# Kernel tuning notes

Hardware: AMD Instinct MI355X
Metric: run time of the kernel (lower is better)

Reference implementation:

```python
import jax, jax.numpy as jnp
import numpy as np

EPS = 1e-9

def setup_inputs() -> dict:
    key = jax.random.key(0)
    k1, k2 = jax.random.split(key)
    h = jax.random.normal(k1, (16384, 4096), dtype=jnp.float32)
    W = jax.random.normal(k2, (64, 4096), dtype=jnp.float32) * 0.02  # nn.Linear weight [n_experts, d]
    return {"h": h, "W": W}

def reference(h, W):
    k = 2
    # logits: [tokens, n_experts]
    logits = jnp.einsum('td,ed->te', h, W)
    weights_full = jax.nn.softmax(logits, axis=-1)
    # top-k on logits (torch.topk returns sorted descending, as does lax.top_k)
    _, idx = jax.lax.top_k(logits, k)  # idx: [tokens, k]
    # masked renormalization: since top-k indices are distinct, the masked sum
    # equals the sum of gathered softmax weights
    gathered = jnp.take_along_axis(weights_full, idx, axis=-1)  # [tokens, k]
    weights_topk = gathered / (jnp.sum(gathered, axis=-1, keepdims=True) + EPS)
    return weights_topk, idx
```

## Files before the change

### kernel.cpp

```cpp
#include <hip/hip_runtime.h>
#include <math.h>

#define DIM   4096
#define NEXP  64
#define MB    32
#define KC    128
#define NST   (DIM / KC)
#define ASTR  (KC + 8)

typedef _Float16 f16x8 __attribute__((ext_vector_type(8)));
typedef _Float16 f16x4 __attribute__((ext_vector_type(4)));
typedef float    f32x4 __attribute__((ext_vector_type(4)));

__global__ __launch_bounds__(256)
void convert_w_kernel(const float* __restrict__ W,
                      _Float16* __restrict__ wh, _Float16* __restrict__ wl) {
    int i = (blockIdx.x * 256 + threadIdx.x) * 4;
    float4 v = *(const float4*)(W + i);
    _Float16 a0 = (_Float16)v.x, a1 = (_Float16)v.y;
    _Float16 a2 = (_Float16)v.z, a3 = (_Float16)v.w;
    f16x4 hh = {a0, a1, a2, a3};
    f16x4 ll = {(_Float16)(v.x - (float)a0), (_Float16)(v.y - (float)a1),
                (_Float16)(v.z - (float)a2), (_Float16)(v.w - (float)a3)};
    *(f16x4*)(wh + i) = hh;
    *(f16x4*)(wl + i) = ll;
}

__global__ __launch_bounds__(256, 2)
void gate_mfma_kernel(const float* __restrict__ h,
                      const _Float16* __restrict__ wh,
                      const _Float16* __restrict__ wl,
                      float* __restrict__ out, int n_tokens) {
    __shared__ _Float16 Ah[2][MB][ASTR];
    __shared__ _Float16 Al[2][MB][ASTR];
    __shared__ float    lg[MB][NEXP + 4];

    const int tid  = threadIdx.x;
    const int lane = tid & 63;
    const int wv   = __builtin_amdgcn_readfirstlane(tid >> 6);
    const int mg   = wv & 1;
    const int ng   = wv >> 1;
    const int t0   = blockIdx.x * MB;
    const int l15  = lane & 15;
    const int quad = lane >> 4;

    const _Float16* bh0 = wh + (size_t)(32 * ng + l15) * DIM + 8 * quad;
    const _Float16* bh1 = bh0 + (size_t)16 * DIM;
    const _Float16* bl0 = wl + (size_t)(32 * ng + l15) * DIM + 8 * quad;
    const _Float16* bl1 = bl0 + (size_t)16 * DIM;

    f32x4 acc0 = {0.f, 0.f, 0.f, 0.f};
    f32x4 acc1 = {0.f, 0.f, 0.f, 0.f};

    float4 st[4];
    int s_t[4], s_q[4];
#pragma unroll
    for (int r = 0; r < 4; ++r) {
        int flat = r * 256 + tid;
        s_t[r] = flat >> 5;
        s_q[r] = flat & 31;
        st[r] = *(const float4*)(h + (size_t)(t0 + s_t[r]) * DIM + 4 * s_q[r]);
    }

    for (int c = 0; c < NST; ++c) {
        const int buf = c & 1;
#pragma unroll
        for (int r = 0; r < 4; ++r) {
            float4 v = st[r];
            _Float16 a0 = (_Float16)v.x, a1 = (_Float16)v.y;
            _Float16 a2 = (_Float16)v.z, a3 = (_Float16)v.w;
            f16x4 hh = {a0, a1, a2, a3};
            f16x4 ll = {(_Float16)(v.x - (float)a0), (_Float16)(v.y - (float)a1),
                        (_Float16)(v.z - (float)a2), (_Float16)(v.w - (float)a3)};
            *(f16x4*)(&Ah[buf][s_t[r]][4 * s_q[r]]) = hh;
            *(f16x4*)(&Al[buf][s_t[r]][4 * s_q[r]]) = ll;
        }
        __syncthreads();

        if (c + 1 < NST) {
            const int kn = (c + 1) * KC;
#pragma unroll
            for (int r = 0; r < 4; ++r)
                st[r] = *(const float4*)(h + (size_t)(t0 + s_t[r]) * DIM + kn + 4 * s_q[r]);
        }

        const _Float16* arow_h = &Ah[buf][16 * mg + l15][8 * quad];
        const _Float16* arow_l = &Al[buf][16 * mg + l15][8 * quad];
        const size_t kb = (size_t)c * KC;
#pragma unroll
        for (int s = 0; s < 4; ++s) {
            f16x8 af_h = *(const f16x8*)(arow_h + 32 * s);
            f16x8 af_l = *(const f16x8*)(arow_l + 32 * s);
            f16x8 b0h  = *(const f16x8*)(bh0 + kb + 32 * s);
            f16x8 b1h  = *(const f16x8*)(bh1 + kb + 32 * s);
            f16x8 b0l  = *(const f16x8*)(bl0 + kb + 32 * s);
            f16x8 b1l  = *(const f16x8*)(bl1 + kb + 32 * s);
            acc0 = __builtin_amdgcn_mfma_f32_16x16x32_f16(af_h, b0h, acc0, 0, 0, 0);
            acc0 = __builtin_amdgcn_mfma_f32_16x16x32_f16(af_h, b0l, acc0, 0, 0, 0);
            acc0 = __builtin_amdgcn_mfma_f32_16x16x32_f16(af_l, b0h, acc0, 0, 0, 0);
            acc1 = __builtin_amdgcn_mfma_f32_16x16x32_f16(af_h, b1h, acc1, 0, 0, 0);
            acc1 = __builtin_amdgcn_mfma_f32_16x16x32_f16(af_h, b1l, acc1, 0, 0, 0);
            acc1 = __builtin_amdgcn_mfma_f32_16x16x32_f16(af_l, b1h, acc1, 0, 0, 0);
        }
    }

#pragma unroll
    for (int r = 0; r < 4; ++r) {
        lg[16 * mg + 4 * quad + r][32 * ng + l15]      = acc0[r];
        lg[16 * mg + 4 * quad + r][32 * ng + 16 + l15] = acc1[r];
    }
    __syncthreads();

    if (tid < MB) {
        const float* row = lg[tid];
        float m = -INFINITY;
#pragma unroll 8
        for (int e = 0; e < NEXP; ++e) m = fmaxf(m, row[e]);
        float z = 0.0f, b1 = -INFINITY, b2 = -INFINITY;
        int i1 = 0, i2 = 0;
        for (int e = 0; e < NEXP; ++e) {
            float v = row[e];
            z += expf(v - m);
            if (v > b1)      { b2 = b1; i2 = i1; b1 = v; i1 = e; }
            else if (v > b2) { b2 = v; i2 = e; }
        }
        float g1 = expf(b1 - m), g2 = expf(b2 - m);
        float w1 = g1 / z, w2 = g2 / z;
        float ssum = w1 + w2 + 1e-9f;
        int t = t0 + tid;
        *(float2*)(out + 2 * t) = make_float2(w1 / ssum, w2 / ssum);
        *(float2*)(out + 2 * n_tokens + 2 * t) = make_float2((float)i1, (float)i2);
    }
}

extern "C" void kernel_launch(void* const* d_in, const int* in_sizes, int n_in,
                              void* d_out, int out_size, void* d_ws, size_t ws_size,
                              hipStream_t stream) {
    const float* h = (const float*)d_in[0];
    const float* W = (const float*)d_in[1];
    float* out = (float*)d_out;
    const int n_tokens = in_sizes[0] / DIM;

    _Float16* wh = (_Float16*)d_ws;
    _Float16* wl = wh + (size_t)NEXP * DIM;

    convert_w_kernel<<<(NEXP * DIM) / (256 * 4), 256, 0, stream>>>(W, wh, wl);
    gate_mfma_kernel<<<n_tokens / MB, 256, 0, stream>>>(h, wh, wl, out, n_tokens);
}
```

Before: 435.4 us.

## Pre-pack W into MFMA fragment order, swizzle LDS, and prefetch B fragments

The weight-conversion kernel now writes W's fp16 hi/lo split in MFMA fragment order, so each lane's B load is one contiguous coalesced 16-byte read. Those fragments are double-buffered in registers one K-chunk ahead. The LDS A tiles drop row padding in favour of an XOR swizzle to avoid bank conflicts. The warp split changes so each wave owns 16 experts and both 16-token M tiles, and occupancy is raised to 3 blocks per CU. The cost is more register pressure from the prefetched B fragments and the unroll, which could limit the higher occupancy target.

Result: faster. 371.6 us (-14.6%).

```diff
diff --git a/kernel.cpp b/kernel.cpp
--- a/kernel.cpp
+++ b/kernel.cpp
@@ -6,74 +6,88 @@
 #define MB    32
 #define KC    128
 #define NST   (DIM / KC)
-#define ASTR  (KC + 8)
 
 typedef _Float16 f16x8 __attribute__((ext_vector_type(8)));
 typedef _Float16 f16x4 __attribute__((ext_vector_type(4)));
 typedef float    f32x4 __attribute__((ext_vector_type(4)));
 
 __global__ __launch_bounds__(256)
-void convert_w_kernel(const float* __restrict__ W,
-                      _Float16* __restrict__ wh, _Float16* __restrict__ wl) {
-    int i = (blockIdx.x * 256 + threadIdx.x) * 4;
-    float4 v = *(const float4*)(W + i);
-    _Float16 a0 = (_Float16)v.x, a1 = (_Float16)v.y;
-    _Float16 a2 = (_Float16)v.z, a3 = (_Float16)v.w;
-    f16x4 hh = {a0, a1, a2, a3};
-    f16x4 ll = {(_Float16)(v.x - (float)a0), (_Float16)(v.y - (float)a1),
-                (_Float16)(v.z - (float)a2), (_Float16)(v.w - (float)a3)};
-    *(f16x4*)(wh + i) = hh;
-    *(f16x4*)(wl + i) = ll;
+void pack_w_kernel(const float* __restrict__ W,
+                   _Float16* __restrict__ wph, _Float16* __restrict__ wpl) {
+    const int flat = blockIdx.x * 256 + threadIdx.x;
+    const int lane = flat & 63;
+    const int ck   = (flat >> 6) & 127;
+    const int nt   = flat >> 13;
+    const int e    = nt * 16 + (lane & 15);
+    const int k0   = ck * 32 + (lane >> 4) * 8;
+    const float* src = W + ((size_t)e << 12) + k0;
+    float4 v0 = *(const float4*)(src);
+    float4 v1 = *(const float4*)(src + 4);
+    float vv[8] = {v0.x, v0.y, v0.z, v0.w, v1.x, v1.y, v1.z, v1.w};
+    f16x8 hi, lo;
+#pragma unroll
+    for (int i = 0; i < 8; ++i) {
+        _Float16 hh = (_Float16)vv[i];
+        hi[i] = hh;
+        lo[i] = (_Float16)(vv[i] - (float)hh);
+    }
+    *(f16x8*)(wph + (size_t)flat * 8) = hi;
+    *(f16x8*)(wpl + (size_t)flat * 8) = lo;
 }
 
-__global__ __launch_bounds__(256, 2)
+__global__ __launch_bounds__(256, 3)
 void gate_mfma_kernel(const float* __restrict__ h,
-                      const _Float16* __restrict__ wh,
-                      const _Float16* __restrict__ wl,
+                      const _Float16* __restrict__ wph,
+                      const _Float16* __restrict__ wpl,
                       float* __restrict__ out, int n_tokens) {
-    __shared__ _Float16 Ah[2][MB][ASTR];
-    __shared__ _Float16 Al[2][MB][ASTR];
+    __shared__ _Float16 Ah[2][MB * KC];
+    __shared__ _Float16 Al[2][MB * KC];
     __shared__ float    lg[MB][NEXP + 4];
 
     const int tid  = threadIdx.x;
     const int lane = tid & 63;
     const int wv   = __builtin_amdgcn_readfirstlane(tid >> 6);
-    const int mg   = wv & 1;
-    const int ng   = wv >> 1;
-    const int t0   = blockIdx.x * MB;
     const int l15  = lane & 15;
     const int quad = lane >> 4;
+    const int t0   = blockIdx.x * MB;
 
-    const _Float16* bh0 = wh + (size_t)(32 * ng + l15) * DIM + 8 * quad;
-    const _Float16* bh1 = bh0 + (size_t)16 * DIM;
-    const _Float16* bl0 = wl + (size_t)(32 * ng + l15) * DIM + 8 * quad;
-    const _Float16* bl1 = bl0 + (size_t)16 * DIM;
-
-    f32x4 acc0 = {0.f, 0.f, 0.f, 0.f};
-    f32x4 acc1 = {0.f, 0.f, 0.f, 0.f};
-
+    int s_t[4], s_q[4];
     float4 st[4];
-    int s_t[4], s_q[4];
 #pragma unroll
     for (int r = 0; r < 4; ++r) {
         int flat = r * 256 + tid;
         s_t[r] = flat >> 5;
         s_q[r] = flat & 31;
-        st[r] = *(const float4*)(h + (size_t)(t0 + s_t[r]) * DIM + 4 * s_q[r]);
+        st[r]  = *(const float4*)(h + (size_t)(t0 + s_t[r]) * DIM + 4 * s_q[r]);
     }
 
+    const _Float16* bph = wph + ((size_t)(wv * 128) * 64 + lane) * 8;
+    const _Float16* bpl = wpl + ((size_t)(wv * 128) * 64 + lane) * 8;
+    f16x8 Bh[2][4], Bl[2][4];
+#pragma unroll
+    for (int s = 0; s < 4; ++s) {
+        Bh[0][s] = *(const f16x8*)(bph + s * 512);
+        Bl[0][s] = *(const f16x8*)(bpl + s * 512);
+    }
+
+    f32x4 acc0 = {0.f, 0.f, 0.f, 0.f};
+    f32x4 acc1 = {0.f, 0.f, 0.f, 0.f};
+
+#pragma unroll 2
     for (int c = 0; c < NST; ++c) {
         const int buf = c & 1;
 #pragma unroll
         for (int r = 0; r < 4; ++r) {
             float4 v = st[r];
-            _Float16 a0 = (_Float16)v.x, a1 = (_Float16)v.y;
-            _Float16 a2 = (_Float16)v.z, a3 = (_Float16)v.w;
+            _Float16 a0 = (_Float16)v.x, a1 = (_Float16)v.y,
+                     a2 = (_Float16)v.z, a3 = (_Float16)v.w;
             f16x4 hh = {a0, a1, a2, a3};
             f16x4 ll = {(_Float16)(v.x - (float)a0), (_Float16)(v.y - (float)a1),
                         (_Float16)(v.z - (float)a2), (_Float16)(v.w - (float)a3)};
-            *(f16x4*)(&Ah[buf][s_t[r]][4 * s_q[r]]) = hh;
-            *(f16x4*)(&Al[buf][s_t[r]][4 * s_q[r]]) = ll;
+            int t = s_t[r], q = s_q[r];
+            int addr = t * KC + (((q >> 1) ^ (t & 15)) << 3) + ((q & 1) << 2);
+            *(f16x4*)(&Ah[buf][addr]) = hh;
+            *(f16x4*)(&Al[buf][addr]) = ll;
         }
         __syncthreads();
 
@@ -82,32 +96,36 @@
 #pragma unroll
             for (int r = 0; r < 4; ++r)
                 st[r] = *(const float4*)(h + (size_t)(t0 + s_t[r]) * DIM + kn + 4 * s_q[r]);
+            const int nb = (c + 1) & 1;
+            const size_t coff = (size_t)(c + 1) * 4 * 512;
+#pragma unroll
+            for (int s = 0; s < 4; ++s) {
+                Bh[nb][s] = *(const f16x8*)(bph + coff + s * 512);
+                Bl[nb][s] = *(const f16x8*)(bpl + coff + s * 512);
+            }
         }
 
-        const _Float16* arow_h = &Ah[buf][16 * mg + l15][8 * quad];
-        const _Float16* arow_l = &Al[buf][16 * mg + l15][8 * quad];
-        const size_t kb = (size_t)c * KC;
 #pragma unroll
         for (int s = 0; s < 4; ++s) {
-            f16x8 af_h = *(const f16x8*)(arow_h + 32 * s);
-            f16x8 af_l = *(const f16x8*)(arow_l + 32 * s);
-            f16x8 b0h  = *(const f16x8*)(bh0 + kb + 32 * s);
-            f16x8 b1h  = *(const f16x8*)(bh1 + kb + 32 * s);
-            f16x8 b0l  = *(const f16x8*)(bl0 + kb + 32 * s);
-            f16x8 b1l  = *(const f16x8*)(bl1 + kb + 32 * s);
-            acc0 = __builtin_amdgcn_mfma_f32_16x16x32_f16(af_h, b0h, acc0, 0, 0, 0);
-            acc0 = __builtin_amdgcn_mfma_f32_16x16x32_f16(af_h, b0l, acc0, 0, 0, 0);
-            acc0 = __builtin_amdgcn_mfma_f32_16x16x32_f16(af_l, b0h, acc0, 0, 0, 0);
-            acc1 = __builtin_amdgcn_mfma_f32_16x16x32_f16(af_h, b1h, acc1, 0, 0, 0);
-            acc1 = __builtin_amdgcn_mfma_f32_16x16x32_f16(af_h, b1l, acc1, 0, 0, 0);
-            acc1 = __builtin_amdgcn_mfma_f32_16x16x32_f16(af_l, b1h, acc1, 0, 0, 0);
+            const int pb = (((4 * s + quad) ^ l15) << 3);
+            f16x8 a0h = *(const f16x8*)(&Ah[buf][l15 * KC + pb]);
+            f16x8 a1h = *(const f16x8*)(&Ah[buf][(16 + l15) * KC + pb]);
+            f16x8 a0l = *(const f16x8*)(&Al[buf][l15 * KC + pb]);
+            f16x8 a1l = *(const f16x8*)(&Al[buf][(16 + l15) * KC + pb]);
+            f16x8 bh = Bh[buf][s], bl = Bl[buf][s];
+            acc0 = __builtin_amdgcn_mfma_f32_16x16x32_f16(a0h, bh, acc0, 0, 0, 0);
+            acc1 = __builtin_amdgcn_mfma_f32_16x16x32_f16(a1h, bh, acc1, 0, 0, 0);
+            acc0 = __builtin_amdgcn_mfma_f32_16x16x32_f16(a0l, bh, acc0, 0, 0, 0);
+            acc1 = __builtin_amdgcn_mfma_f32_16x16x32_f16(a1l, bh, acc1, 0, 0, 0);
+            acc0 = __builtin_amdgcn_mfma_f32_16x16x32_f16(a0h, bl, acc0, 0, 0, 0);
+            acc1 = __builtin_amdgcn_mfma_f32_16x16x32_f16(a1h, bl, acc1, 0, 0, 0);
         }
     }
 
 #pragma unroll
     for (int r = 0; r < 4; ++r) {
-        lg[16 * mg + 4 * quad + r][32 * ng + l15]      = acc0[r];
-        lg[16 * mg + 4 * quad + r][32 * ng + 16 + l15] = acc1[r];
+        lg[4 * quad + r][wv * 16 + l15]      = acc0[r];
+        lg[16 + 4 * quad + r][wv * 16 + l15] = acc1[r];
     }
     __syncthreads();
 
@@ -141,9 +159,9 @@
     float* out = (float*)d_out;
     const int n_tokens = in_sizes[0] / DIM;
 
-    _Float16* wh = (_Float16*)d_ws;
-    _Float16* wl = wh + (size_t)NEXP * DIM;
+    _Float16* wph = (_Float16*)d_ws;
+    _Float16* wpl = wph + (size_t)NEXP * DIM;
 
-    convert_w_kernel<<<(NEXP * DIM) / (256 * 4), 256, 0, stream>>>(W, wh, wl);
-    gate_mfma_kernel<<<n_tokens / MB, 256, 0, stream>>>(h, wh, wl, out, n_tokens);
+    pack_w_kernel<<<(NEXP * DIM / 8) / 256, 256, 0, stream>>>(W, wph, wpl);
+    gate_mfma_kernel<<<n_tokens / MB, 256, 0, stream>>>(h, wph, wpl, out, n_tokens);
 }
```
